# Kernel optimization log

Measured on AMD Instinct MI355X. Metric: run time of the kernel, lower is better.

## Reference

```python
import math
import jax, jax.numpy as jnp
import numpy as np

B, S, H, DQ, DV = 2, 2048, 16, 192, 128
NEG_INF = jnp.float32(-1e30)


def setup_inputs() -> dict:
    key = jax.random.key(0)
    kq, kk, kv = jax.random.split(key, 3)
    q = jax.random.normal(kq, (B, S, H, DQ), dtype=jnp.float32)
    k = jax.random.normal(kk, (B, S, H, DQ), dtype=jnp.float32)
    v = jax.random.normal(kv, (B, S, H, DV), dtype=jnp.float32)
    return {"q": q, "k": k, "v": v}


def reference(q, k, v):
    # Causal MLA attention, BSHD layout, asymmetric QK vs V head dims.
    dq = q.shape[-1]
    scale = jnp.asarray(math.sqrt(1.0 / dq), dtype=q.dtype)  # default 1/sqrt(dq)
    # scores: [B, H, S, S]
    scores = jnp.einsum("bqhd,bkhd->bhqk", q, k) * scale
    s = q.shape[1]
    causal = jnp.tril(jnp.ones((s, s), dtype=bool))  # qidx >= kidx
    scores = jnp.where(causal[None, None, :, :], scores, NEG_INF)
    p = jax.nn.softmax(scores, axis=-1)
    # out: [B, S, H, DV]
    out = jnp.einsum("bhqk,bkhd->bqhd", p, v)
    return out
```

## Files before the change

### kernel.cpp

```cpp
#include <hip/hip_runtime.h>

#define B_ 2
#define S_ 2048
#define H_ 16
#define DQ_ 192
#define DV_ 128
#define SCL2 0.10411163731422901f

typedef short short8 __attribute__((ext_vector_type(8)));
typedef float f32x4 __attribute__((ext_vector_type(4)));
typedef float f32x16 __attribute__((ext_vector_type(16)));
typedef unsigned uint2v __attribute__((ext_vector_type(2)));

#define KG_BYTES ((size_t)25165824)
#define VG_BYTES ((size_t)16777216)

__device__ __forceinline__ unsigned short f2bf(float f) {
  union { float f; unsigned u; } x; x.f = f;
  unsigned r = x.u + 0x7FFFu + ((x.u >> 16) & 1u);
  return (unsigned short)(r >> 16);
}

__device__ __forceinline__ float hw_exp2(float x) {
  float r; asm("v_exp_f32 %0, %1" : "=v"(r) : "v"(x)); return r;
}
__device__ __forceinline__ unsigned cvtpk(float lo, float hi) {
  unsigned r; asm("v_cvt_pk_bf16_f32 %0, %1, %2" : "=v"(r) : "v"(lo), "v"(hi)); return r;
}
__device__ __forceinline__ float pl32max(float x) {
  uint2v r = __builtin_amdgcn_permlane32_swap(__float_as_uint(x), __float_as_uint(x), false, false);
  return fmaxf(__uint_as_float(r[0]), __uint_as_float(r[1]));
}
__device__ __forceinline__ float pl32add(float x) {
  uint2v r = __builtin_amdgcn_permlane32_swap(__float_as_uint(x), __float_as_uint(x), false, false);
  return __uint_as_float(r[0]) + __uint_as_float(r[1]);
}

#define GLL16(src, dst) \
  __builtin_amdgcn_global_load_lds((const __attribute__((address_space(1))) void*)(src), \
                                   (__attribute__((address_space(3))) void*)(dst), 16, 0, 0)

__global__ __launch_bounds__(256) void prep_k(const float* __restrict__ K,
                                              unsigned short* __restrict__ Kg) {
  int idx = blockIdx.x * 256 + threadIdx.x;
  int d4 = idx % 48; int r = idx / 48;
  int h = r % H_; r /= H_;
  int s = r % S_; int b = r / S_;
  float4 f = *(const float4*)(K + (size_t)((b * S_ + s) * H_ + h) * DQ_ + d4 * 4);
  ushort4 u; u.x = f2bf(f.x); u.y = f2bf(f.y); u.z = f2bf(f.z); u.w = f2bf(f.w);
  size_t rowb = (size_t)((b * H_ + h) * S_ + s) * (DQ_ * 2);
  int cb = (d4 * 8) ^ ((s & 7) << 4);
  *(ushort4*)((char*)Kg + rowb + cb) = u;
}

__global__ __launch_bounds__(256) void prep_v(const float* __restrict__ V,
                                              unsigned short* __restrict__ Vg) {
  __shared__ float lv[64][132];
  int blk = blockIdx.x;
  int tile = blk & 31, bh = blk >> 5;
  int b = bh >> 4, h = bh & 15;
  int tid = threadIdx.x;
  #pragma unroll
  for (int it = 0; it < 8; ++it) {
    int idx = it * 256 + tid;
    int s_in = idx >> 5, d4 = idx & 31;
    float4 f = *(const float4*)(V + (size_t)((b * S_ + tile * 64 + s_in) * H_ + h) * DV_ + d4 * 4);
    lv[s_in][d4 * 4 + 0] = f.x; lv[s_in][d4 * 4 + 1] = f.y;
    lv[s_in][d4 * 4 + 2] = f.z; lv[s_in][d4 * 4 + 3] = f.w;
  }
  __syncthreads();
  char* base = (char*)Vg + (size_t)blk * 16384;
  #pragma unroll
  for (int it = 0; it < 4; ++it) {
    int ch = it * 256 + tid;
    int pr = ch >> 4, ci = ch & 15;
    int orig = ci ^ (pr & 15);
    int dv = pr * 2 + (orig >> 3);
    int k0 = (orig & 7) * 8;
    short8 u;
    #pragma unroll
    for (int e = 0; e < 8; ++e) u[e] = (short)f2bf(lv[k0 + e][dv]);
    *(short8*)(base + ch * 16) = u;
  }
}

__launch_bounds__(256, 2)
__global__ void mla_fwd(const float* __restrict__ Q,
                        const unsigned short* __restrict__ Kg,
                        const unsigned short* __restrict__ Vg,
                        float* __restrict__ O) {
  __shared__ __align__(16) unsigned char SB[2][40960];

  const int tid  = threadIdx.x;
  const int wid  = tid >> 6;
  const int lane = tid & 63;
  const int l31  = lane & 31;
  const int hi   = lane >> 5;
  const int hi16 = hi * 16;
  const int qg   = wid & 1;
  const int kh   = wid >> 1;

  const int i  = blockIdx.x;
  const int x  = i & 7;
  const int li = i >> 3;
  const int bh = x * 4 + (li >> 4);
  const int jj = li & 15;
  const int b  = bh >> 4, h = bh & 15;

  const char* kg_bh = (const char*)Kg + (size_t)bh * S_ * (DQ_ * 2);
  const char* vg_bh = (const char*)Vg + (size_t)bh * 32 * 16384;

  const int kxor = (lane & 7) << 4;
  const int prl  = l31 >> 1;
  const int nb_  = (lane & 1) * 8 + hi;
  int voff[2];
  #pragma unroll
  for (int ks = 0; ks < 2; ++ks) {
    int n = nb_ + kh * 4 + ks * 2;
    voff[ks] = prl * 256 + ((n ^ prl) << 4);
  }

  #define STAGE(buf)                                                       \
    do {                                                                   \
      _Pragma("unroll")                                                    \
      for (int ci = 0; ci < 10; ++ci) {                                    \
        const int cc = wid * 10 + ci;                                      \
        const char* src = (cc < 24) ? (kS + ci * 1024) : (vS + ci * 1024); \
        GLL16(src, &SB[buf][cc * 1024]);                                   \
      }                                                                    \
    } while (0)

  for (int job = 0; job < 2; ++job) {
    const int qt  = job ? jj : (31 - jj);
    const int wq0 = qt * 64 + qg * 32;
    const int qln = wq0 + l31;

    short8 qf[12];
    {
      const size_t qoff = (size_t)((b * S_ + qln) * H_ + h) * DQ_;
      #pragma unroll
      for (int d0 = 0; d0 < 12; ++d0) {
        const float* p = Q + qoff + d0 * 16 + hi * 8;
        float4 f0 = *(const float4*)(p);
        float4 f1 = *(const float4*)(p + 4);
        short8 a;
        a[0] = f2bf(f0.x * SCL2); a[1] = f2bf(f0.y * SCL2);
        a[2] = f2bf(f0.z * SCL2); a[3] = f2bf(f0.w * SCL2);
        a[4] = f2bf(f1.x * SCL2); a[5] = f2bf(f1.y * SCL2);
        a[6] = f2bf(f1.z * SCL2); a[7] = f2bf(f1.w * SCL2);
        qf[d0] = a;
      }
    }

    f32x16 o4[4];
    #pragma unroll
    for (int t2 = 0; t2 < 4; ++t2) o4[t2] = (f32x16)0.0f;
    float m = -1e30f, l = 0.0f;

    const int ntiles = qt + 1;

    const char* kS = kg_bh + wid * 10240 + lane * 16;
    const char* vS = vg_bh - 24576 + wid * 10240 + lane * 16;

    STAGE(0); kS += 24576; vS += 16384;
    __syncthreads();

    int cur = 0;
    for (int kt = 0; kt < ntiles; ++kt) {
      const int kbase = kt * 64;
      const int khb = kbase + kh * 32;
      if (kt + 1 < ntiles) { STAGE(cur ^ 1); kS += 24576; vS += 16384; }

      if (khb <= wq0 + 31) {
        const char* kr = (const char*)&SB[cur][0] + (kh * 32 + l31) * 384;
        f32x16 s = (f32x16)0.0f;
        __builtin_amdgcn_s_setprio(1);
        #pragma unroll
        for (int d0 = 0; d0 < 12; ++d0) {
          const int col = (d0 * 32 + hi16) ^ kxor;
          s = __builtin_amdgcn_mfma_f32_32x32x16_bf16(*(const short8*)(kr + col), qf[d0], s, 0, 0, 0);
        }
        __builtin_amdgcn_s_setprio(0);

        const char* vb = (const char*)&SB[cur][0] + 24576;
        short8 v00 = *(const short8*)(vb + 0 * 4096 + voff[0]);
        short8 v01 = *(const short8*)(vb + 0 * 4096 + voff[1]);
        short8 v10 = *(const short8*)(vb + 1 * 4096 + voff[0]);
        short8 v11 = *(const short8*)(vb + 1 * 4096 + voff[1]);
        short8 v20 = *(const short8*)(vb + 2 * 4096 + voff[0]);
        short8 v21 = *(const short8*)(vb + 2 * 4096 + voff[1]);
        short8 v30 = *(const short8*)(vb + 3 * 4096 + voff[0]);
        short8 v31 = *(const short8*)(vb + 3 * 4096 + voff[1]);

        float p_[16];
        #pragma unroll
        for (int r = 0; r < 16; ++r) p_[r] = s[r];
        if (khb + 31 > wq0) {
          const int rem = qln - khb - 4 * hi;
          #pragma unroll
          for (int r = 0; r < 16; ++r) {
            const int kof = (r & 3) + 8 * (r >> 2);
            if (kof > rem) p_[r] = -1e30f;
          }
        }

        float t8[8];
        #pragma unroll
        for (int r = 0; r < 8; ++r) t8[r] = fmaxf(p_[r], p_[8 + r]);
        float t4[4];
        #pragma unroll
        for (int r = 0; r < 4; ++r) t4[r] = fmaxf(t8[r], t8[4 + r]);
        float mx = fmaxf(fmaxf(t4[0], t4[1]), fmaxf(t4[2], t4[3]));
        mx = pl32max(mx);
        if (__any(mx > m + 8.0f)) {
          float mn = fmaxf(m, mx);
          float al = hw_exp2(m - mn);
          #pragma unroll
          for (int t2 = 0; t2 < 4; ++t2) o4[t2] *= al;
          l *= al; m = mn;
        }
        #pragma unroll
        for (int rr = 0; rr < 16; ++rr) p_[rr] = hw_exp2(p_[rr] - m);
        float a8[8];
        #pragma unroll
        for (int r = 0; r < 8; ++r) a8[r] = p_[r] + p_[8 + r];
        float a4[4];
        #pragma unroll
        for (int r = 0; r < 4; ++r) a4[r] = a8[r] + a8[4 + r];
        l += (a4[0] + a4[1]) + (a4[2] + a4[3]);

        unsigned a_ = cvtpk(p_[0], p_[1]),   b2_ = cvtpk(p_[2], p_[3]);
        unsigned c_ = cvtpk(p_[4], p_[5]),   d_  = cvtpk(p_[6], p_[7]);
        unsigned e_ = cvtpk(p_[8], p_[9]),   f_  = cvtpk(p_[10], p_[11]);
        unsigned g_ = cvtpk(p_[12], p_[13]), h_  = cvtpk(p_[14], p_[15]);
        uint2v s02 = __builtin_amdgcn_permlane32_swap(a_, c_, false, false);
        uint2v s13 = __builtin_amdgcn_permlane32_swap(b2_, d_, false, false);
        uint2v s46 = __builtin_amdgcn_permlane32_swap(e_, g_, false, false);
        uint2v s57 = __builtin_amdgcn_permlane32_swap(f_, h_, false, false);
        union { unsigned u[4]; short8 s; } pb0, pb1;
        pb0.u[0] = s02[0]; pb0.u[1] = s13[0]; pb0.u[2] = s02[1]; pb0.u[3] = s13[1];
        pb1.u[0] = s46[0]; pb1.u[1] = s57[0]; pb1.u[2] = s46[1]; pb1.u[3] = s57[1];

        __builtin_amdgcn_s_setprio(1);
        o4[0] = __builtin_amdgcn_mfma_f32_32x32x16_bf16(v00, pb0.s, o4[0], 0, 0, 0);
        o4[0] = __builtin_amdgcn_mfma_f32_32x32x16_bf16(v01, pb1.s, o4[0], 0, 0, 0);
        o4[1] = __builtin_amdgcn_mfma_f32_32x32x16_bf16(v10, pb0.s, o4[1], 0, 0, 0);
        o4[1] = __builtin_amdgcn_mfma_f32_32x32x16_bf16(v11, pb1.s, o4[1], 0, 0, 0);
        o4[2] = __builtin_amdgcn_mfma_f32_32x32x16_bf16(v20, pb0.s, o4[2], 0, 0, 0);
        o4[2] = __builtin_amdgcn_mfma_f32_32x32x16_bf16(v21, pb1.s, o4[2], 0, 0, 0);
        o4[3] = __builtin_amdgcn_mfma_f32_32x32x16_bf16(v30, pb0.s, o4[3], 0, 0, 0);
        o4[3] = __builtin_amdgcn_mfma_f32_32x32x16_bf16(v31, pb1.s, o4[3], 0, 0, 0);
        __builtin_amdgcn_s_setprio(0);
      }

      __syncthreads();
      cur ^= 1;
    }

    float lr = pl32add(l);
    char* mrg = (char*)&SB[0][0];
    if (kh == 1) {
      float* po = (float*)(mrg + qg * 17408 + lane * 272);
      #pragma unroll
      for (int t2 = 0; t2 < 4; ++t2) {
        #pragma unroll
        for (int rr = 0; rr < 4; ++rr) {
          float4 st = { o4[t2][rr * 4 + 0], o4[t2][rr * 4 + 1],
                        o4[t2][rr * 4 + 2], o4[t2][rr * 4 + 3] };
          *(float4*)(po + t2 * 16 + rr * 4) = st;
        }
      }
      float* pm = (float*)(mrg + 34816 + (qg * 64 + lane) * 8);
      pm[0] = m; pm[1] = lr;
    }
    __syncthreads();
    if (kh == 0) {
      const float* po = (const float*)(mrg + qg * 17408 + lane * 272);
      const float* pm = (const float*)(mrg + 34816 + (qg * 64 + lane) * 8);
      const float mB = pm[0], lB = pm[1];
      const float ms = fmaxf(m, mB);
      const float wA = hw_exp2(m - ms), wB = hw_exp2(mB - ms);
      const float inv = 1.0f / (lr * wA + lB * wB);
      float* ob = O + (size_t)((b * S_ + qln) * H_ + h) * DV_;
      #pragma unroll
      for (int t2 = 0; t2 < 4; ++t2) {
        #pragma unroll
        for (int rr = 0; rr < 4; ++rr) {
          float4 vb4 = *(const float4*)(po + t2 * 16 + rr * 4);
          float4 st = { (o4[t2][rr * 4 + 0] * wA + vb4.x * wB) * inv,
                        (o4[t2][rr * 4 + 1] * wA + vb4.y * wB) * inv,
                        (o4[t2][rr * 4 + 2] * wA + vb4.z * wB) * inv,
                        (o4[t2][rr * 4 + 3] * wA + vb4.w * wB) * inv };
          *(float4*)(ob + t2 * 32 + rr * 8 + hi * 4) = st;
        }
      }
    }
    __syncthreads();
  }
  #undef STAGE
}

__launch_bounds__(256)
__global__ void mla_fwd_fb(const float* __restrict__ Q,
                           const float* __restrict__ K,
                           const float* __restrict__ V,
                           float* __restrict__ O) {
  __shared__ __align__(16) unsigned short Kl[2][32][200];
  __shared__ __align__(16) unsigned short Vt[2][128][40];
  __shared__ __align__(16) unsigned short Pl[4][16][40];
  const int tid = threadIdx.x, wid = tid >> 6, lane = tid & 63;
  const int l15 = lane & 15, g = lane >> 4;
  const int qtile = (int)gridDim.x - 1 - (int)blockIdx.x;
  const int bh = blockIdx.y, b = bh >> 4, h = bh & 15;
  const int q0w = qtile * 64 + wid * 16;
  const int krs = H_ * DQ_, vrs = H_ * DV_;
  short8 aq[6];
  {
    const int qoff = ((b * S_ + (q0w + l15)) * H_ + h) * DQ_;
    #pragma unroll
    for (int d0 = 0; d0 < 6; ++d0) {
      const float* p = Q + qoff + d0 * 32 + g * 8;
      float4 f0 = *(const float4*)(p); float4 f1 = *(const float4*)(p + 4);
      short8 a;
      a[0]=f2bf(f0.x); a[1]=f2bf(f0.y); a[2]=f2bf(f0.z); a[3]=f2bf(f0.w);
      a[4]=f2bf(f1.x); a[5]=f2bf(f1.y); a[6]=f2bf(f1.z); a[7]=f2bf(f1.w);
      aq[d0] = a;
    }
  }
  f32x4 o[8];
  #pragma unroll
  for (int t = 0; t < 8; ++t) o[t] = (f32x4)0.0f;
  float m[4], l[4];
  #pragma unroll
  for (int r = 0; r < 4; ++r) { m[r] = -1e30f; l[r] = 0.0f; }
  const int ntiles = qtile * 2 + 2;
  float4 kr[6], vr[4];
  {
    const float* Kb = K + ((b * S_) * H_ + h) * DQ_;
    #pragma unroll
    for (int i = 0; i < 6; ++i) { int idx = i*256+tid; int row = idx/48, c4 = idx%48;
      kr[i] = *(const float4*)(Kb + row*krs + c4*4); }
    const float* Vb = V + ((b * S_) * H_ + h) * DV_;
    #pragma unroll
    for (int i = 0; i < 4; ++i) { int idx = i*256+tid; int row = idx&31, c4 = idx>>5;
      vr[i] = *(const float4*)(Vb + row*vrs + c4*4); }
    #pragma unroll
    for (int i = 0; i < 6; ++i) { int idx = i*256+tid; int row = idx/48, c4 = idx%48;
      ushort4 u; u.x=f2bf(kr[i].x); u.y=f2bf(kr[i].y); u.z=f2bf(kr[i].z); u.w=f2bf(kr[i].w);
      *(ushort4*)&Kl[0][row][c4*4] = u; }
    #pragma unroll
    for (int i = 0; i < 4; ++i) { int idx = i*256+tid; int row = idx&31, c4 = idx>>5;
      Vt[0][c4*4+0][row]=f2bf(vr[i].x); Vt[0][c4*4+1][row]=f2bf(vr[i].y);
      Vt[0][c4*4+2][row]=f2bf(vr[i].z); Vt[0][c4*4+3][row]=f2bf(vr[i].w); }
  }
  __syncthreads();
  int cur = 0;
  for (int kt = 0; kt < ntiles; ++kt) {
    const int kbase = kt * 32;
    const bool pf = (kt + 1 < ntiles);
    if (pf) {
      const int nb = kbase + 32;
      const float* Kb = K + ((b*S_+nb)*H_ + h)*DQ_;
      #pragma unroll
      for (int i = 0; i < 6; ++i) { int idx = i*256+tid; int row = idx/48, c4 = idx%48;
        kr[i] = *(const float4*)(Kb + row*krs + c4*4); }
      const float* Vb = V + ((b*S_+nb)*H_ + h)*DV_;
      #pragma unroll
      for (int i = 0; i < 4; ++i) { int idx = i*256+tid; int row = idx&31, c4 = idx>>5;
        vr[i] = *(const float4*)(Vb + row*vrs + c4*4); }
    }
    f32x4 sa0 = (f32x4)0.0f, sa1 = (f32x4)0.0f;
    #pragma unroll
    for (int d0 = 0; d0 < 6; ++d0) {
      short8 b0 = *(const short8*)&Kl[cur][l15][d0*32 + g*8];
      sa0 = __builtin_amdgcn_mfma_f32_16x16x32_bf16(aq[d0], b0, sa0, 0, 0, 0);
      short8 b1 = *(const short8*)&Kl[cur][16+l15][d0*32 + g*8];
      sa1 = __builtin_amdgcn_mfma_f32_16x16x32_bf16(aq[d0], b1, sa1, 0, 0, 0);
    }
    float p0[4], p1[4];
    #pragma unroll
    for (int r = 0; r < 4; ++r) {
      const int qg = q0w + 4*g + r;
      float s0 = sa0[r]*SCL2, s1 = sa1[r]*SCL2;
      if (kbase + l15 > qg) s0 = -1e30f;
      if (kbase + 16 + l15 > qg) s1 = -1e30f;
      p0[r] = s0; p1[r] = s1;
    }
    #pragma unroll
    for (int r = 0; r < 4; ++r) {
      float rm = fmaxf(p0[r], p1[r]);
      #pragma unroll
      for (int off = 1; off < 16; off <<= 1) rm = fmaxf(rm, __shfl_xor(rm, off));
      float mn = fmaxf(m[r], rm);
      float alpha = exp2f(m[r] - mn); m[r] = mn;
      float e0 = exp2f(p0[r] - mn), e1 = exp2f(p1[r] - mn);
      p0[r] = e0; p1[r] = e1;
      float rsum = e0 + e1;
      #pragma unroll
      for (int off = 1; off < 16; off <<= 1) rsum += __shfl_xor(rsum, off);
      l[r] = l[r]*alpha + rsum;
      #pragma unroll
      for (int t = 0; t < 8; ++t) o[t][r] *= alpha;
    }
    #pragma unroll
    for (int r = 0; r < 4; ++r) {
      Pl[wid][4*g+r][l15]      = f2bf(p0[r]);
      Pl[wid][4*g+r][16+l15]   = f2bf(p1[r]);
    }
    short8 pa = *(const short8*)&Pl[wid][l15][g*8];
    #pragma unroll
    for (int t = 0; t < 8; ++t) {
      short8 vb = *(const short8*)&Vt[cur][t*16+l15][g*8];
      o[t] = __builtin_amdgcn_mfma_f32_16x16x32_bf16(pa, vb, o[t], 0, 0, 0);
    }
    if (pf) {
      #pragma unroll
      for (int i = 0; i < 6; ++i) { int idx = i*256+tid; int row = idx/48, c4 = idx%48;
        ushort4 u; u.x=f2bf(kr[i].x); u.y=f2bf(kr[i].y); u.z=f2bf(kr[i].z); u.w=f2bf(kr[i].w);
        *(ushort4*)&Kl[cur^1][row][c4*4] = u; }
      #pragma unroll
      for (int i = 0; i < 4; ++i) { int idx = i*256+tid; int row = idx&31, c4 = idx>>5;
        Vt[cur^1][c4*4+0][row]=f2bf(vr[i].x); Vt[cur^1][c4*4+1][row]=f2bf(vr[i].y);
        Vt[cur^1][c4*4+2][row]=f2bf(vr[i].z); Vt[cur^1][c4*4+3][row]=f2bf(vr[i].w); }
    }
    __syncthreads();
    cur ^= 1;
  }
  #pragma unroll
  for (int r = 0; r < 4; ++r) {
    const int qg = q0w + 4*g + r;
    const float inv = 1.0f / l[r];
    #pragma unroll
    for (int t = 0; t < 8; ++t)
      O[((b*S_+qg)*H_ + h)*DV_ + t*16 + l15] = o[t][r] * inv;
  }
}

extern "C" void kernel_launch(void* const* d_in, const int* in_sizes, int n_in,
                              void* d_out, int out_size, void* d_ws, size_t ws_size,
                              hipStream_t stream) {
  const float* q = (const float*)d_in[0];
  const float* k = (const float*)d_in[1];
  const float* v = (const float*)d_in[2];
  float* out = (float*)d_out;

  if (ws_size >= KG_BYTES + VG_BYTES) {
    unsigned short* Kg = (unsigned short*)d_ws;
    unsigned short* Vg = (unsigned short*)((char*)d_ws + KG_BYTES);
    prep_k<<<dim3((B_ * S_ * H_ * 48) / 256), dim3(256), 0, stream>>>(k, Kg);
    prep_v<<<dim3(B_ * H_ * 32), dim3(256), 0, stream>>>(v, Vg);
    mla_fwd<<<dim3(512), dim3(256), 0, stream>>>(q, Kg, Vg, out);
  } else {
    dim3 grid(S_ / 64, B_ * H_);
    mla_fwd_fb<<<grid, dim3(256), 0, stream>>>(q, k, v, out);
  }
}
```

Measured before the change: 91.53 us.

## Use 512-thread blocks with 128-row Q tiles and triple-buffered K/V staging

Doubles the workgroup to 8 waves covering 128 query rows per block, so each staged K/V tile is shared by twice as many waves and the grid is halved. Replaces double buffering plus a block-wide sync per tile with a three-deep LDS ring, vmcnt-based waits and a bare s_barrier, prefetching two tiles ahead. This aims to cut global/LDS traffic per query and hide load latency, at the cost of one block per CU, more LDS, and coarser causal work balance.

New measurement: 90.77 us. Within noise of the previous version (-0.8%).

```diff
diff --git a/kernel.cpp b/kernel.cpp
--- a/kernel.cpp
+++ b/kernel.cpp
@@ -84,12 +84,12 @@
   }
 }
 
-__launch_bounds__(256, 2)
+__launch_bounds__(512, 1)
 __global__ void mla_fwd(const float* __restrict__ Q,
                         const unsigned short* __restrict__ Kg,
                         const unsigned short* __restrict__ Vg,
                         float* __restrict__ O) {
-  __shared__ __align__(16) unsigned char SB[2][40960];
+  __shared__ __align__(16) unsigned char SB[3][40960];
 
   const int tid  = threadIdx.x;
   const int wid  = tid >> 6;
@@ -97,14 +97,14 @@
   const int l31  = lane & 31;
   const int hi   = lane >> 5;
   const int hi16 = hi * 16;
-  const int qg   = wid & 1;
-  const int kh   = wid >> 1;
+  const int qg   = wid & 3;
+  const int kh   = wid >> 2;
 
   const int i  = blockIdx.x;
   const int x  = i & 7;
   const int li = i >> 3;
-  const int bh = x * 4 + (li >> 4);
-  const int jj = li & 15;
+  const int bh = x * 4 + (li >> 3);
+  const int jj = li & 7;
   const int b  = bh >> 4, h = bh & 15;
 
   const char* kg_bh = (const char*)Kg + (size_t)bh * S_ * (DQ_ * 2);
@@ -120,19 +120,21 @@
     voff[ks] = prl * 256 + ((n ^ prl) << 4);
   }
 
-  #define STAGE(buf)                                                       \
-    do {                                                                   \
-      _Pragma("unroll")                                                    \
-      for (int ci = 0; ci < 10; ++ci) {                                    \
-        const int cc = wid * 10 + ci;                                      \
-        const char* src = (cc < 24) ? (kS + ci * 1024) : (vS + ci * 1024); \
-        GLL16(src, &SB[buf][cc * 1024]);                                   \
-      }                                                                    \
+  #define STAGE(buf, t)                                                           \
+    do {                                                                          \
+      const char* kba = kg_bh + (size_t)(t) * 24576 + wid * 5120 + lane * 16;     \
+      const char* vba = vg_bh + (size_t)(t) * 16384 - 24576 + wid * 5120 + lane * 16; \
+      _Pragma("unroll")                                                           \
+      for (int ci = 0; ci < 5; ++ci) {                                            \
+        const int cc = wid * 5 + ci;                                              \
+        const char* src = (cc < 24) ? (kba + ci * 1024) : (vba + ci * 1024);      \
+        GLL16(src, &SB[buf][cc * 1024]);                                          \
+      }                                                                           \
     } while (0)
 
   for (int job = 0; job < 2; ++job) {
-    const int qt  = job ? jj : (31 - jj);
-    const int wq0 = qt * 64 + qg * 32;
+    const int qt  = job ? jj : (15 - jj);
+    const int wq0 = qt * 128 + qg * 32;
     const int qln = wq0 + l31;
 
     short8 qf[12];
@@ -157,22 +159,26 @@
     for (int t2 = 0; t2 < 4; ++t2) o4[t2] = (f32x16)0.0f;
     float m = -1e30f, l = 0.0f;
 
-    const int ntiles = qt + 1;
-
-    const char* kS = kg_bh + wid * 10240 + lane * 16;
-    const char* vS = vg_bh - 24576 + wid * 10240 + lane * 16;
-
-    STAGE(0); kS += 24576; vS += 16384;
-    __syncthreads();
-
-    int cur = 0;
+    const int ntiles = 2 * qt + 2;
+
+    STAGE(0, 0);
+    if (ntiles > 1) STAGE(1, 1);
+
+    int bc = 0;
     for (int kt = 0; kt < ntiles; ++kt) {
+      if (kt + 1 < ntiles) asm volatile("s_waitcnt vmcnt(10)" ::: "memory");
+      else                 asm volatile("s_waitcnt vmcnt(0)" ::: "memory");
+      __builtin_amdgcn_s_barrier();
+      if (kt + 2 < ntiles) {
+        int bs = bc - 1; if (bs < 0) bs = 2;
+        STAGE(bs, kt + 2);
+      }
+
       const int kbase = kt * 64;
       const int khb = kbase + kh * 32;
-      if (kt + 1 < ntiles) { STAGE(cur ^ 1); kS += 24576; vS += 16384; }
 
       if (khb <= wq0 + 31) {
-        const char* kr = (const char*)&SB[cur][0] + (kh * 32 + l31) * 384;
+        const char* kr = (const char*)&SB[bc][0] + (kh * 32 + l31) * 384;
         f32x16 s = (f32x16)0.0f;
         __builtin_amdgcn_s_setprio(1);
         #pragma unroll
@@ -182,7 +188,7 @@
         }
         __builtin_amdgcn_s_setprio(0);
 
-        const char* vb = (const char*)&SB[cur][0] + 24576;
+        const char* vb = (const char*)&SB[bc][0] + 24576;
         short8 v00 = *(const short8*)(vb + 0 * 4096 + voff[0]);
         short8 v01 = *(const short8*)(vb + 0 * 4096 + voff[1]);
         short8 v10 = *(const short8*)(vb + 1 * 4096 + voff[0]);
@@ -253,11 +259,11 @@
         __builtin_amdgcn_s_setprio(0);
       }
 
-      __syncthreads();
-      cur ^= 1;
+      ++bc; if (bc == 3) bc = 0;
     }
 
     float lr = pl32add(l);
+    __syncthreads();
     char* mrg = (char*)&SB[0][0];
     if (kh == 1) {
       float* po = (float*)(mrg + qg * 17408 + lane * 272);
@@ -270,13 +276,13 @@
           *(float4*)(po + t2 * 16 + rr * 4) = st;
         }
       }
-      float* pm = (float*)(mrg + 34816 + (qg * 64 + lane) * 8);
+      float* pm = (float*)(mrg + 69632 + (qg * 64 + lane) * 8);
       pm[0] = m; pm[1] = lr;
     }
     __syncthreads();
     if (kh == 0) {
       const float* po = (const float*)(mrg + qg * 17408 + lane * 272);
-      const float* pm = (const float*)(mrg + 34816 + (qg * 64 + lane) * 8);
+      const float* pm = (const float*)(mrg + 69632 + (qg * 64 + lane) * 8);
       const float mB = pm[0], lB = pm[1];
       const float ms = fmaxf(m, mB);
       const float wA = hw_exp2(m - ms), wB = hw_exp2(mB - ms);
@@ -449,7 +455,7 @@
     unsigned short* Vg = (unsigned short*)((char*)d_ws + KG_BYTES);
     prep_k<<<dim3((B_ * S_ * H_ * 48) / 256), dim3(256), 0, stream>>>(k, Kg);
     prep_v<<<dim3(B_ * H_ * 32), dim3(256), 0, stream>>>(v, Vg);
-    mla_fwd<<<dim3(512), dim3(256), 0, stream>>>(q, Kg, Vg, out);
+    mla_fwd<<<dim3(256), dim3(512), 0, stream>>>(q, Kg, Vg, out);
   } else {
     dim3 grid(S_ / 64, B_ * H_);
     mla_fwd_fb<<<grid, dim3(256), 0, stream>>>(q, k, v, out);
```
